# Optimization experiments

Measured on AMD Instinct MI355X. Metric: run time of the kernel, lower is better.

The kernel has to match this reference:

```python
import jax, jax.numpy as jnp
import numpy as np

B, N, DIM = 2, 512, 512
HEADS, DIM_HEAD, MAX_LEN = 8, 64, 1024


def _skew(QEr):
    # pad last dim on the left by 1, reshape (n, n+1) -> (n+1, n), drop first row
    padded = jnp.pad(QEr, ((0, 0), (0, 0), (0, 0), (1, 0)))
    b, h, r, c = padded.shape
    return padded.reshape(b, h, c, r)[:, :, 1:, :]


def _fft_multiply_parallel(A, x):
    # A: [b,h,n,n] decay matrix; x: [b,h,n,d]
    b, h, n, d = x.shape
    # y = [last column of A, first row of A] -> [b,h,2n]
    y = jnp.concatenate([A[:, :, :, -1], A[:, :, 0, :]], axis=-1)
    v = jnp.concatenate([x, jnp.zeros_like(x)], axis=-2)  # zero-pad rows n -> 2n
    # Faithful to the original torch code: fftn over ALL axes (incl. batch/head),
    # then ifft over the LAST axis only, then slice back to n rows.
    H = jnp.fft.fftn(y)[:, :, :, None] * jnp.fft.fftn(v)
    return jnp.fft.ifft(H)[:, :, :n, :]


def _forward(x, Wq, Wk, Wv, Er):
    b, n, _ = x.shape

    def split_heads(t):
        return t.reshape(b, n, HEADS, DIM_HEAD).transpose(0, 2, 1, 3)  # [b,h,n,d]

    q = split_heads(x @ Wq)
    k = split_heads(x @ Wk)
    v = split_heads(x @ Wv)
    # global (Frobenius) norm over the full tensor, as torch.norm(t)
    q = q / jnp.linalg.norm(q)
    k = k / jnp.linalg.norm(k)
    q_ = jax.nn.elu(q)
    k_ = jax.nn.elu(k)

    Er_t = Er[MAX_LEN - n:, :].T        # [d, n]
    QEr = q @ Er_t                       # [b,h,n,n]
    c = jnp.exp(_skew(QEr))              # relative-position decay, [b,h,n,n]

    a_1 = jnp.einsum('bhnx,bhny->bhnxy', k_, v).reshape(b, HEADS, n, DIM_HEAD * DIM_HEAD)
    d_2 = _fft_multiply_parallel(c, k_)                                   # [b,h,n,d] complex
    d_1 = _fft_multiply_parallel(c, a_1).reshape(b, HEADS, n, DIM_HEAD, DIM_HEAD)

    top = jnp.einsum('bhnx,bhnyz->bhnz', q_, d_1)    # complex [b,h,n,d]
    bottom = jnp.einsum('bhnx,bhny->bhny', q_, d_2)  # complex [b,h,n,d]
    return top / bottom


def setup_inputs() -> dict:
    key = jax.random.key(0)
    k1, k2, k3, k4, k5 = jax.random.split(key, 5)
    s = jnp.float32(1.0 / np.sqrt(DIM))
    return {
        'x': jax.random.normal(k1, (B, N, DIM), dtype=jnp.float32),
        'Wq': jax.random.normal(k2, (DIM, HEADS * DIM_HEAD), dtype=jnp.float32) * s,
        'Wk': jax.random.normal(k3, (DIM, HEADS * DIM_HEAD), dtype=jnp.float32) * s,
        'Wv': jax.random.normal(k4, (DIM, HEADS * DIM_HEAD), dtype=jnp.float32) * s,
        'Er': jax.random.normal(k5, (MAX_LEN, DIM_HEAD), dtype=jnp.float32),
    }


def reference(x, Wq, Wk, Wv, Er):
    return _forward(x, Wq, Wk, Wv, Er)
```

## Files before the change

kernel.cpp:

```cpp
#include <hip/hip_runtime.h>
#include <math.h>


#define DIMX 512
#define NPOS 512
#define PADIDX(m) ((m) + ((m) >> 4))

typedef unsigned short ushort_t;
typedef unsigned int uint_t;
typedef __bf16 bf16x8 __attribute__((ext_vector_type(8)));
typedef float floatx4 __attribute__((ext_vector_type(4)));

static __device__ inline ushort_t f2bf(float f) {
    uint_t u = __float_as_uint(f);
    u = u + 0x7FFFu + ((u >> 16) & 1u);
    return (ushort_t)(u >> 16);
}
static __device__ inline float bf2f(ushort_t h) {
    return __uint_as_float(((uint_t)h) << 16);
}

#define BFLY(lo, hi, tw) do {                                   \
    const float sr_ = (lo).x - (hi).x, si_ = (lo).y - (hi).y;   \
    (lo).x += (hi).x; (lo).y += (hi).y;                         \
    (hi).x = sr_ * (tw).x - si_ * (tw).y;                       \
    (hi).y = sr_ * (tw).y + si_ * (tw).x;                       \
} while (0)

__global__ __launch_bounds__(256)
void conv_kernel(const float* __restrict__ x,
                 const float* __restrict__ Wk, const float* __restrict__ Wv,
                 ushort_t* __restrict__ xh, ushort_t* __restrict__ xl,
                 ushort_t* __restrict__ wth, ushort_t* __restrict__ wtl,
                 float2* __restrict__ twd)
{
    const int blk = blockIdx.x;
    const int t = threadIdx.x;
    if (blk < 512) {
        const int idx4 = blk * 256 + t;
        const float4 v = ((const float4*)x)[idx4];
        const float vf[4] = {v.x, v.y, v.z, v.w};
        ushort_t h[4], l[4];
        #pragma unroll
        for (int e = 0; e < 4; ++e) {
            h[e] = f2bf(vf[e]);
            l[e] = f2bf(vf[e] - bf2f(h[e]));
        }
        const ushort4 hv4 = make_ushort4(h[0], h[1], h[2], h[3]);
        const ushort4 lv4 = make_ushort4(l[0], l[1], l[2], l[3]);
        *(ushort4*)(xh + (size_t)idx4 * 4) = hv4;
        *(ushort4*)(xl + (size_t)idx4 * 4) = lv4;
    } else if (blk < 1024) {
        __shared__ float tile[32][33];
        const int b2 = blk - 512;
        const int s  = b2 >> 8;
        const int kt = (b2 >> 4) & 15;
        const int nt = b2 & 15;
        const int c  = t & 31, r4 = t >> 5;
        const float* __restrict__ W = s ? Wv : Wk;
        #pragma unroll
        for (int i = 0; i < 4; ++i) {
            const int row = r4 + i * 8;
            tile[row][c] = W[(size_t)(kt * 32 + row) * 512 + nt * 32 + c];
        }
        __syncthreads();
        #pragma unroll
        for (int i = 0; i < 4; ++i) {
            const int nl = r4 + i * 8;
            const float v = tile[c][nl];
            const ushort_t h = f2bf(v);
            const ushort_t l = f2bf(v - bf2f(h));
            const size_t o = (size_t)(s * 512 + nt * 32 + nl) * 512 + kt * 32 + c;
            wth[o] = h;
            wtl[o] = l;
        }
    } else {
        const int jj = (blk - 1024) * 256 + t;
        double s, cc;
        sincos(-6.2831853071795864769 * (double)jj / 1024.0, &s, &cc);
        twd[jj] = make_float2((float)cc, (float)s);
    }
}

__global__ __launch_bounds__(256)
void gemm_mfma_kernel(const ushort_t* __restrict__ xh, const ushort_t* __restrict__ xl,
                      const ushort_t* __restrict__ wth, const ushort_t* __restrict__ wtl,
                      float* __restrict__ K, float* __restrict__ V,
                      float* __restrict__ partials)
{
    const int blk = blockIdx.x;
    const int ct = blk >> 5;
    const int rt = blk & 31;
    const int t = threadIdx.x;
    const int w = t >> 6, lane = t & 63;
    const int qd = lane >> 4, lm = lane & 15;
    const int mrow  = rt * 32 + (w >> 1) * 16 + lm;
    const int ncol0 = ct * 64 + (w & 1) * 32;
    const size_t aoff  = (size_t)mrow * 512 + qd * 8;
    const size_t boff0 = (size_t)(ncol0 + lm) * 512 + qd * 8;
    const size_t boff1 = (size_t)(ncol0 + 16 + lm) * 512 + qd * 8;

    floatx4 acc0 = {0.f, 0.f, 0.f, 0.f};
    floatx4 acc1 = {0.f, 0.f, 0.f, 0.f};

    #pragma unroll
    for (int ks = 0; ks < 16; ++ks) {
        const int k0 = ks * 32;
        const bf16x8 Ah  = *(const bf16x8*)&xh [aoff  + k0];
        const bf16x8 Al  = *(const bf16x8*)&xl [aoff  + k0];
        const bf16x8 B0h = *(const bf16x8*)&wth[boff0 + k0];
        const bf16x8 B0l = *(const bf16x8*)&wtl[boff0 + k0];
        const bf16x8 B1h = *(const bf16x8*)&wth[boff1 + k0];
        const bf16x8 B1l = *(const bf16x8*)&wtl[boff1 + k0];
        acc0 = __builtin_amdgcn_mfma_f32_16x16x32_bf16(Ah, B0h, acc0, 0, 0, 0);
        acc0 = __builtin_amdgcn_mfma_f32_16x16x32_bf16(Ah, B0l, acc0, 0, 0, 0);
        acc0 = __builtin_amdgcn_mfma_f32_16x16x32_bf16(Al, B0h, acc0, 0, 0, 0);
        acc1 = __builtin_amdgcn_mfma_f32_16x16x32_bf16(Ah, B1h, acc1, 0, 0, 0);
        acc1 = __builtin_amdgcn_mfma_f32_16x16x32_bf16(Ah, B1l, acc1, 0, 0, 0);
        acc1 = __builtin_amdgcn_mfma_f32_16x16x32_bf16(Al, B1h, acc1, 0, 0, 0);
    }

    __shared__ float red[4];
    float ss = 0.f;
    const int orow0 = rt * 32 + (w >> 1) * 16 + qd * 4;
    float* __restrict__ O = (ct < 8) ? K : V;
    const int cb = (ct < 8) ? 0 : 512;
    const int c0 = ncol0 + lm - cb;
    #pragma unroll
    for (int r = 0; r < 4; ++r) {
        const size_t row = orow0 + r;
        const float v0 = acc0[r], v1 = acc1[r];
        O[row * 512 + c0]      = v0;
        O[row * 512 + c0 + 16] = v1;
        if (ct < 8) ss += v0 * v0 + v1 * v1;
    }
    #pragma unroll
    for (int off = 32; off > 0; off >>= 1)
        ss += __shfl_down(ss, off, 64);
    if (lane == 0) red[w] = ss;
    __syncthreads();
    if (t == 0) partials[blk] = red[0] + red[1] + red[2] + red[3];
}

__device__ __constant__ float C8[8] = {
    1.f, 0.70710678118654752440f, 0.f, -0.70710678118654752440f,
   -1.f, -0.70710678118654752440f, 0.f, 0.70710678118654752440f };
__device__ __constant__ float S8[8] = {
    0.f, -0.70710678118654752440f, -1.f, -0.70710678118654752440f,
    0.f,  0.70710678118654752440f,  1.f,  0.70710678118654752440f };

__global__ __launch_bounds__(256)
void stage1_kernel(const float* __restrict__ K,
                   const float* __restrict__ V,
                   const float* __restrict__ partials,
                   float2* __restrict__ Gk,
                   float2* __restrict__ Gp)
{
    const int m = blockIdx.x;
    const int t = threadIdx.x;
    __shared__ float kk[2][8][64];
    __shared__ float pp[2][8][64];
    __shared__ float skp[16][4];
    __shared__ float sk[2][8];
    __shared__ float sred[4];

    float p = partials[t] + partials[t + 256];
    #pragma unroll
    for (int off = 32; off > 0; off >>= 1)
        p += __shfl_down(p, off, 64);
    if ((t & 63) == 0) sred[t >> 6] = p;
    __syncthreads();
    const float scale = (float)(1.0 / sqrt((double)sred[0] + (double)sred[1] +
                                           (double)sred[2] + (double)sred[3]));

    {
        const int e0 = t * 4;
        const int b = e0 >> 9, rem = e0 & 511, h = rem >> 6, z = rem & 63;
        const size_t src = (size_t)(b * 512 + m) * DIMX + h * 64 + z;
        const float4 kv4 = *(const float4*)&K[src];
        const float4 vv4 = *(const float4*)&V[src];
        const float kf[4] = {kv4.x, kv4.y, kv4.z, kv4.w};
        const float vf[4] = {vv4.x, vv4.y, vv4.z, vv4.w};
        #pragma unroll
        for (int e = 0; e < 4; ++e) {
            const float kv = kf[e] * scale;
            kk[b][h][z + e] = kv > 0.f ? kv : expm1f(kv);
            pp[b][h][z + e] = vf[e];
        }
    }
    __syncthreads();
    if (t < 64) {
        const int bh = t >> 2, q = t & 3;
        float s = 0.f;
        #pragma unroll
        for (int zz = 0; zz < 16; ++zz) s += kk[bh >> 3][bh & 7][q * 16 + zz];
        skp[bh][q] = s;
    }
    __syncthreads();
    if (t < 16) sk[t >> 3][t & 7] = skp[t][0] + skp[t][1] + skp[t][2] + skp[t][3];
    __syncthreads();

    for (int e2 = t; e2 < 512; e2 += 256) {
        const int be = e2 >> 5;
        const int zp = e2 & 31;
        const int beta = be >> 3, eta = be & 7;
        float kr[2] = {0.f, 0.f}, ki[2] = {0.f, 0.f};
        float pr[2] = {0.f, 0.f}, pim[2] = {0.f, 0.f};
        #pragma unroll
        for (int b = 0; b < 2; ++b) {
            const float sgn = (beta & b) ? -1.f : 1.f;
            #pragma unroll
            for (int h = 0; h < 8; ++h) {
                const int ph = (eta * h) & 7;
                const float cr = C8[ph], ci = S8[ph];
                const float skv = sk[b][h];
                #pragma unroll
                for (int zz = 0; zz < 2; ++zz) {
                    const int z = zp * 2 + zz;
                    const float a = kk[b][h][z] * sgn;
                    kr[zz] = fmaf(a, cr, kr[zz]);
                    ki[zz] = fmaf(a, ci, ki[zz]);
                    const float p2 = (pp[b][h][z] * skv) * sgn;
                    pr[zz]  = fmaf(p2, cr, pr[zz]);
                    pim[zz] = fmaf(p2, ci, pim[zz]);
                }
            }
        }
        const float4 rk = make_float4(kr[0], ki[0], kr[1], ki[1]);
        const float4 rp = make_float4(pr[0], pim[0], pr[1], pim[1]);
        const size_t o = ((size_t)be * NPOS + m) * 64 + zp * 2;
        *(float4*)&Gk[o] = rk;
        *(float4*)&Gp[o] = rp;
    }
}

__global__ __launch_bounds__(256)
void fft_div_kernel(const float2* __restrict__ Gk,
                    const float2* __restrict__ Gp,
                    const float2* __restrict__ twd,
                    float* __restrict__ out, int out_cplx)
{
    const int blk = blockIdx.x;
    const int j  = blk & 7;
    const int l  = (blk >> 3) & 3;
    const int be = blk >> 5;
    const int zg = j * 4 + l;
    const int t  = threadIdx.x;

    __shared__ float2 g[4][1088];
    __shared__ float2 w[544];

    for (int jj = t; jj < 512; jj += 256)
        w[PADIDX(jj)] = twd[jj];
    __syncthreads();

    for (int e = t; e < 1024; e += 256) {
        const int a = e >> 9;
        const int m = e & 511;
        const float4 v4 = *(const float4*)&(a ? Gp : Gk)[((size_t)be * NPOS + m) * 64 + zg * 2];
        const float2 v0 = make_float2(v4.x, v4.y);
        const float2 v1 = make_float2(v4.z, v4.w);
        const float2 tw = w[PADIDX(m)];
        g[a * 2 + 0][PADIDX(m)] = v0;
        g[a * 2 + 1][PADIDX(m)] = v1;
        g[a * 2 + 0][PADIDX(m + 512)] = make_float2(v0.x * tw.x - v0.y * tw.y,
                                                    v0.x * tw.y + v0.y * tw.x);
        g[a * 2 + 1][PADIDX(m + 512)] = make_float2(v1.x * tw.x - v1.y * tw.y,
                                                    v1.x * tw.y + v1.y * tw.x);
    }
    __syncthreads();

    const int wv   = t >> 6;
    const int lane = t & 63;

    #pragma unroll
    for (int q = 0; q < 2; ++q) {
        const int arr = wv;
        const int h   = q;
        const int jo  = lane;
        float2 f[8];
        #pragma unroll
        for (int k = 0; k < 8; ++k)
            f[k] = g[arr][PADIDX(h * 512 + jo + k * 64)];
        #pragma unroll
        for (int k = 0; k < 4; ++k) {
            const float2 tw = w[PADIDX(2 * jo + 128 * k)];
            BFLY(f[k], f[k + 4], tw);
        }
        {
            const float2 tw0 = w[PADIDX(4 * jo)];
            const float2 tw1 = w[PADIDX(4 * jo + 256)];
            BFLY(f[0], f[2], tw0); BFLY(f[1], f[3], tw1);
            BFLY(f[4], f[6], tw0); BFLY(f[5], f[7], tw1);
        }
        {
            const float2 tw = w[PADIDX(8 * jo)];
            BFLY(f[0], f[1], tw); BFLY(f[2], f[3], tw);
            BFLY(f[4], f[5], tw); BFLY(f[6], f[7], tw);
        }
        #pragma unroll
        for (int k = 0; k < 8; ++k)
            g[arr][PADIDX(h * 512 + jo + k * 64)] = f[k];
    }

    #pragma unroll
    for (int q = 0; q < 2; ++q) {
        const int arr = wv;
        const int b64 = q * 8 + (lane >> 3);
        const int jo  = lane & 7;
        const int e0  = b64 * 64 + jo;
        float2 f[8];
        #pragma unroll
        for (int k = 0; k < 8; ++k)
            f[k] = g[arr][PADIDX(e0 + 8 * k)];
        #pragma unroll
        for (int k = 0; k < 4; ++k) {
            const float2 tw = w[PADIDX(16 * jo + 128 * k)];
            BFLY(f[k], f[k + 4], tw);
        }
        {
            const float2 tw0 = w[PADIDX(32 * jo)];
            const float2 tw1 = w[PADIDX(32 * jo + 256)];
            BFLY(f[0], f[2], tw0); BFLY(f[1], f[3], tw1);
            BFLY(f[4], f[6], tw0); BFLY(f[5], f[7], tw1);
        }
        {
            const float2 tw = w[PADIDX(64 * jo)];
            BFLY(f[0], f[1], tw); BFLY(f[2], f[3], tw);
            BFLY(f[4], f[5], tw); BFLY(f[6], f[7], tw);
        }
        #pragma unroll
        for (int k = 0; k < 8; ++k)
            g[arr][PADIDX(e0 + 8 * k)] = f[k];
    }

    #pragma unroll
    for (int q = 0; q < 2; ++q) {
        const int arr = wv;
        const int b8  = q * 64 + lane;
        const int e0  = b8 * 8;
        float2 f[8];
        #pragma unroll
        for (int k = 0; k < 8; ++k)
            f[k] = g[arr][PADIDX(e0 + k)];
        BFLY(f[0], f[4], w[PADIDX(0)]);
        BFLY(f[1], f[5], w[PADIDX(128)]);
        BFLY(f[2], f[6], w[PADIDX(256)]);
        BFLY(f[3], f[7], w[PADIDX(384)]);
        {
            const float2 tw0 = w[PADIDX(0)];
            const float2 tw1 = w[PADIDX(256)];
            BFLY(f[0], f[2], tw0); BFLY(f[1], f[3], tw1);
            BFLY(f[4], f[6], tw0); BFLY(f[5], f[7], tw1);
        }
        f[0].x += f[1].x; f[0].y += f[1].y;
        f[2].x += f[3].x; f[2].y += f[3].y;
        f[4].x += f[5].x; f[4].y += f[5].y;
        f[6].x += f[7].x; f[6].y += f[7].y;
        g[arr][PADIDX(e0 + 0)] = f[0];
        g[arr][PADIDX(e0 + 2)] = f[2];
        g[arr][PADIDX(e0 + 4)] = f[4];
        g[arr][PADIDX(e0 + 6)] = f[6];
    }
    __syncthreads();

    for (int e2 = t; e2 < 512; e2 += 256) {
        const int i  = e2;
        const int pi = PADIDX(2 * i);
        const int mu = (int)(__brev((unsigned)i) >> 23);
        float4 res;
        #pragma unroll
        for (int zi = 0; zi < 2; ++zi) {
            const float2 D  = g[zi][pi];
            const float2 Nm = g[2 + zi][pi];
            const float inv = 1.f / (D.x * D.x + D.y * D.y);
            const float rr = (Nm.x * D.x + Nm.y * D.y) * inv;
            const float ri = (Nm.y * D.x - Nm.x * D.y) * inv;
            if (zi == 0) { res.x = rr; res.y = ri; }
            else         { res.z = rr; res.w = ri; }
        }
        const size_t o = ((size_t)be * NPOS + mu) * 64 + zg * 2;
        if (out_cplx) {
            *(float4*)&((float2*)out)[o] = res;
        } else {
            out[o]     = res.x;
            out[o + 1] = res.z;
        }
    }
}

__global__ __launch_bounds__(256)
void gemm_kv_kernel(const float* __restrict__ x,
                    const float* __restrict__ Wk,
                    const float* __restrict__ Wv,
                    float* __restrict__ K,
                    float* __restrict__ V,
                    float* __restrict__ partials)
{
    const int blk  = blockIdx.x;
    const int sel  = (blk >> 2) & 1;
    const int cg2  = blk & 3;
    const int rt   = blk >> 3;
    const int row0 = rt * 16;
    const int col0 = cg2 * 128;
    const int t    = threadIdx.x;
    const int tc   = t & 31;
    const int tr   = t >> 5;
    const float* __restrict__ W   = sel ? Wv : Wk;
    float* __restrict__       Out = sel ? V  : K;

    __shared__ float xs[16][DIMX];
    __shared__ float red[4];

    #pragma unroll
    for (int jj = 0; jj < 8; ++jj) {
        const int f = t + jj * 256;
        const int row = f >> 7, c4 = f & 127;
        *(float4*)&xs[row][c4 * 4] = *(const float4*)&x[(size_t)(row0 + row) * DIMX + c4 * 4];
    }
    __syncthreads();

    const float* Wb = W + col0 + tc * 4;
    float4 wA[8], wB[8];
    #pragma unroll
    for (int jj = 0; jj < 8; ++jj) wA[jj] = *(const float4*)&Wb[(size_t)(jj) * DIMX];
    #pragma unroll
    for (int jj = 0; jj < 8; ++jj) wB[jj] = *(const float4*)&Wb[(size_t)(8 + jj) * DIMX];

    float acc[2][4] = {{0,0,0,0},{0,0,0,0}};
    const int r0 = tr * 2;

    #define COMPUTE_CHUNK(WREG, CH)                                            \
        {   float4 xv0a = *(const float4*)&xs[r0][(CH) * 8];                   \
            float4 xv0b = *(const float4*)&xs[r0][(CH) * 8 + 4];               \
            float4 xv1a = *(const float4*)&xs[r0 + 1][(CH) * 8];               \
            float4 xv1b = *(const float4*)&xs[r0 + 1][(CH) * 8 + 4];           \
            _Pragma("unroll")                                                  \
            for (int kk = 0; kk < 4; ++kk) {                                   \
                const float x0 = (&xv0a.x)[kk], x1 = (&xv1a.x)[kk];            \
                _Pragma("unroll")                                              \
                for (int cc = 0; cc < 4; ++cc) {                               \
                    acc[0][cc] = fmaf(x0, (&WREG[kk].x)[cc], acc[0][cc]);      \
                    acc[1][cc] = fmaf(x1, (&WREG[kk].x)[cc], acc[1][cc]);      \
                } }                                                            \
            _Pragma("unroll")                                                  \
            for (int kk = 0; kk < 4; ++kk) {                                   \
                const float x0 = (&xv0b.x)[kk], x1 = (&xv1b.x)[kk];            \
                _Pragma("unroll")                                              \
                for (int cc = 0; cc < 4; ++cc) {                               \
                    acc[0][cc] = fmaf(x0, (&WREG[kk + 4].x)[cc], acc[0][cc]);  \
                    acc[1][cc] = fmaf(x1, (&WREG[kk + 4].x)[cc], acc[1][cc]);  \
                } } }

    for (int ch = 0; ch < 64; ch += 2) {
        COMPUTE_CHUNK(wA, ch)
        if (ch < 62) {
            #pragma unroll
            for (int jj = 0; jj < 8; ++jj)
                wA[jj] = *(const float4*)&Wb[(size_t)((ch + 2) * 8 + jj) * DIMX];
        }
        COMPUTE_CHUNK(wB, ch + 1)
        if (ch < 62) {
            #pragma unroll
            for (int jj = 0; jj < 8; ++jj)
                wB[jj] = *(const float4*)&Wb[(size_t)((ch + 3) * 8 + jj) * DIMX];
        }
    }
    #undef COMPUTE_CHUNK

    float ss = 0.f;
    #pragma unroll
    for (int i = 0; i < 2; ++i) {
        const int row = row0 + r0 + i;
        const float4 o = make_float4(acc[i][0], acc[i][1], acc[i][2], acc[i][3]);
        *(float4*)&Out[(size_t)row * DIMX + col0 + tc * 4] = o;
        ss += o.x * o.x + o.y * o.y + o.z * o.z + o.w * o.w;
    }
    if (sel == 0) {
        #pragma unroll
        for (int off = 32; off > 0; off >>= 1)
            ss += __shfl_down(ss, off, 64);
        if ((t & 63) == 0) red[t >> 6] = ss;
        __syncthreads();
        if (t == 0) partials[blk] = red[0] + red[1] + red[2] + red[3];
    } else {
        if (t == 0) partials[blk] = 0.f;
    }
}

__global__ __launch_bounds__(256)
void mdft_fallback_kernel(const float2* __restrict__ Gk,
                          const float2* __restrict__ Gp,
                          float* __restrict__ out,
                          int out_cplx)
{
    const int blk = blockIdx.x;
    const int be = blk >> 6, z = blk & 63;
    const int t = threadIdx.x;
    __shared__ float2 gk[512];
    __shared__ float2 gp[512];
    __shared__ float2 w[1024];

    for (int m = t; m < 512; m += 256) {
        const size_t idx = ((size_t)be * NPOS + m) * 64 + z;
        gk[m] = Gk[idx];
        gp[m] = Gp[idx];
    }
    for (int jj = t; jj < 1024; jj += 256) {
        double s, c;
        sincos(-6.2831853071795864769 * (double)jj / 1024.0, &s, &c);
        w[jj] = make_float2((float)c, (float)s);
    }
    __syncthreads();

    #pragma unroll
    for (int half = 0; half < 2; ++half) {
        const int mu = t + half * 256;
        double dr = 0.0, di = 0.0, nr = 0.0, ni = 0.0;
        int idx = 0;
        for (int m = 0; m < 512; ++m) {
            const float2 tw = w[idx];
            idx = (idx + mu) & 1023;
            const float2 a = gk[m];
            dr += (double)(a.x * tw.x - a.y * tw.y);
            di += (double)(a.x * tw.y + a.y * tw.x);
            const float2 p2 = gp[m];
            nr += (double)(p2.x * tw.x - p2.y * tw.y);
            ni += (double)(p2.x * tw.y + p2.y * tw.x);
        }
        const double dmag = dr * dr + di * di;
        const double orr = (nr * dr + ni * di) / dmag;
        const double oii = (ni * dr - nr * di) / dmag;
        const size_t o = ((size_t)be * NPOS + mu) * 64 + z;
        if (out_cplx) {
            out[2 * o]     = (float)orr;
            out[2 * o + 1] = (float)oii;
        } else {
            out[o] = (float)orr;
        }
    }
}

extern "C" void kernel_launch(void* const* d_in, const int* in_sizes, int n_in,
                              void* d_out, int out_size, void* d_ws, size_t ws_size,
                              hipStream_t stream)
{
    const float* x  = (const float*)d_in[0];
    const float* Wk = (const float*)d_in[2];
    const float* Wv = (const float*)d_in[3];
    float* out = (float*)d_out;

    char* ws = (char*)d_ws;
    float*  K    = (float*)(ws);
    float*  V    = (float*)(ws + (size_t)2097152);
    float2* Gk   = (float2*)(ws + (size_t)4194304);
    float*  part = (float*)(ws + (size_t)8388608);
    const int out_cplx = (out_size >= 2 * 2 * 8 * 512 * 64) ? 1 : 0;

    const bool ws_big = (ws_size >= (size_t)20971520);
    float2* Gp = ws_big ? (float2*)(ws + (size_t)8390656)
                        : (float2*)d_out;

    if (ws_big) {
        ushort_t* xh  = (ushort_t*)(ws + (size_t)16777216);
        ushort_t* xl  = (ushort_t*)(ws + (size_t)17825792);
        ushort_t* wth = (ushort_t*)(ws + (size_t)18874368);
        ushort_t* wtl = (ushort_t*)(ws + (size_t)19922944);
        float2*   twd = (float2*)(ws + (size_t)12584960);
        hipLaunchKernelGGL(conv_kernel, dim3(1026), dim3(256), 0, stream,
                           x, Wk, Wv, xh, xl, wth, wtl, twd);
        hipLaunchKernelGGL(gemm_mfma_kernel, dim3(512), dim3(256), 0, stream,
                           xh, xl, wth, wtl, K, V, part);
        hipLaunchKernelGGL(stage1_kernel, dim3(512), dim3(256), 0, stream,
                           K, V, part, Gk, Gp);
        hipLaunchKernelGGL(fft_div_kernel, dim3(512), dim3(256), 0, stream,
                           Gk, Gp, twd, out, out_cplx);
    } else {
        hipLaunchKernelGGL(gemm_kv_kernel, dim3(512), dim3(256), 0, stream,
                           x, Wk, Wv, K, V, part);
        hipLaunchKernelGGL(stage1_kernel, dim3(512), dim3(256), 0, stream,
                           K, V, part, Gk, Gp);
        hipLaunchKernelGGL(mdft_fallback_kernel, dim3(1024), dim3(256), 0, stream,
                           Gk, Gp, out, out_cplx);
    }
}
```

Measured before the change: 105.4 us.

## Stage GEMM weight tiles in LDS with async loads; fuse FFT pre-twiddle

The projection GEMM now brings each block's shared weight tile into double-buffered LDS through global_load_lds. All four waves read the tile from there, where before each wave loaded it redundantly from global memory, and the wave-to-tile mapping is reorganised to match. The FFT-divide kernel no longer stores a pre-twiddled upper half at load time. The first radix stage now reads the lower half and applies the twiddle in registers, handling the twiddled half first so the in-place writes are safe. This removes one LDS write pass and one barrier, at the cost of added barriers per k-step in the GEMM.

After: 100.1 us. 5.0% less time.

```diff
diff --git a/kernel.cpp b/kernel.cpp
--- a/kernel.cpp
+++ b/kernel.cpp
@@ -94,38 +94,62 @@
     const int t = threadIdx.x;
     const int w = t >> 6, lane = t & 63;
     const int qd = lane >> 4, lm = lane & 15;
-    const int mrow  = rt * 32 + (w >> 1) * 16 + lm;
-    const int ncol0 = ct * 64 + (w & 1) * 32;
-    const size_t aoff  = (size_t)mrow * 512 + qd * 8;
-    const size_t boff0 = (size_t)(ncol0 + lm) * 512 + qd * 8;
-    const size_t boff1 = (size_t)(ncol0 + 16 + lm) * 512 + qd * 8;
+
+    const int mrow = rt * 32 + (w & 1) * 16 + lm;
+    const int wcol = (w >> 1) * 32;
+    const size_t aoff = (size_t)mrow * 512 + qd * 8;
+
+    __shared__ __align__(16) ushort_t Bs[2][2][8][64][8];
+    __shared__ float red[4];
+
+    #define STAGE(buf_, k0_)                                                     \
+    {                                                                            \
+        _Pragma("unroll")                                                        \
+        for (int i = 0; i < 4; ++i) {                                            \
+            const int seg = w * 4 + i;                                           \
+            const int arr_ = seg >> 3, kq_ = seg & 7;                            \
+            const ushort_t* src_ = (arr_ ? wtl : wth)                            \
+                + (size_t)(ct * 64 + lane) * 512 + (k0_) + kq_ * 8;              \
+            __builtin_amdgcn_global_load_lds(                                    \
+                (const __attribute__((address_space(1))) uint_t*)src_,           \
+                (__attribute__((address_space(3))) uint_t*)&Bs[buf_][arr_][kq_][0][0], \
+                16, 0, 0);                                                       \
+        }                                                                        \
+    }
 
     floatx4 acc0 = {0.f, 0.f, 0.f, 0.f};
     floatx4 acc1 = {0.f, 0.f, 0.f, 0.f};
 
-    #pragma unroll
-    for (int ks = 0; ks < 16; ++ks) {
-        const int k0 = ks * 32;
-        const bf16x8 Ah  = *(const bf16x8*)&xh [aoff  + k0];
-        const bf16x8 Al  = *(const bf16x8*)&xl [aoff  + k0];
-        const bf16x8 B0h = *(const bf16x8*)&wth[boff0 + k0];
-        const bf16x8 B0l = *(const bf16x8*)&wtl[boff0 + k0];
-        const bf16x8 B1h = *(const bf16x8*)&wth[boff1 + k0];
-        const bf16x8 B1l = *(const bf16x8*)&wtl[boff1 + k0];
-        acc0 = __builtin_amdgcn_mfma_f32_16x16x32_bf16(Ah, B0h, acc0, 0, 0, 0);
-        acc0 = __builtin_amdgcn_mfma_f32_16x16x32_bf16(Ah, B0l, acc0, 0, 0, 0);
-        acc0 = __builtin_amdgcn_mfma_f32_16x16x32_bf16(Al, B0h, acc0, 0, 0, 0);
-        acc1 = __builtin_amdgcn_mfma_f32_16x16x32_bf16(Ah, B1h, acc1, 0, 0, 0);
-        acc1 = __builtin_amdgcn_mfma_f32_16x16x32_bf16(Ah, B1l, acc1, 0, 0, 0);
-        acc1 = __builtin_amdgcn_mfma_f32_16x16x32_bf16(Al, B1h, acc1, 0, 0, 0);
-    }
-
-    __shared__ float red[4];
+    STAGE(0, 0)
+    for (int ks = 0; ks < 8; ++ks) {
+        __syncthreads();
+        const int buf = ks & 1;
+        const int k0 = ks * 64;
+        if (ks < 7) STAGE(buf ^ 1, k0 + 64)
+        #pragma unroll
+        for (int s2 = 0; s2 < 2; ++s2) {
+            const bf16x8 Ah = *(const bf16x8*)&xh[aoff + k0 + s2 * 32];
+            const bf16x8 Al = *(const bf16x8*)&xl[aoff + k0 + s2 * 32];
+            const int kq = s2 * 4 + qd;
+            const bf16x8 B0h = *(const bf16x8*)Bs[buf][0][kq][wcol + lm];
+            const bf16x8 B0l = *(const bf16x8*)Bs[buf][1][kq][wcol + lm];
+            const bf16x8 B1h = *(const bf16x8*)Bs[buf][0][kq][wcol + 16 + lm];
+            const bf16x8 B1l = *(const bf16x8*)Bs[buf][1][kq][wcol + 16 + lm];
+            acc0 = __builtin_amdgcn_mfma_f32_16x16x32_bf16(Ah, B0h, acc0, 0, 0, 0);
+            acc0 = __builtin_amdgcn_mfma_f32_16x16x32_bf16(Ah, B0l, acc0, 0, 0, 0);
+            acc0 = __builtin_amdgcn_mfma_f32_16x16x32_bf16(Al, B0h, acc0, 0, 0, 0);
+            acc1 = __builtin_amdgcn_mfma_f32_16x16x32_bf16(Ah, B1h, acc1, 0, 0, 0);
+            acc1 = __builtin_amdgcn_mfma_f32_16x16x32_bf16(Ah, B1l, acc1, 0, 0, 0);
+            acc1 = __builtin_amdgcn_mfma_f32_16x16x32_bf16(Al, B1h, acc1, 0, 0, 0);
+        }
+    }
+    #undef STAGE
+
     float ss = 0.f;
-    const int orow0 = rt * 32 + (w >> 1) * 16 + qd * 4;
+    const int orow0 = rt * 32 + (w & 1) * 16 + qd * 4;
     float* __restrict__ O = (ct < 8) ? K : V;
     const int cb = (ct < 8) ? 0 : 512;
-    const int c0 = ncol0 + lm - cb;
+    const int c0 = ct * 64 + wcol + lm - cb;
     #pragma unroll
     for (int r = 0; r < 4; ++r) {
         const size_t row = orow0 + r;
@@ -252,21 +276,12 @@
 
     for (int jj = t; jj < 512; jj += 256)
         w[PADIDX(jj)] = twd[jj];
-    __syncthreads();
-
     for (int e = t; e < 1024; e += 256) {
         const int a = e >> 9;
         const int m = e & 511;
         const float4 v4 = *(const float4*)&(a ? Gp : Gk)[((size_t)be * NPOS + m) * 64 + zg * 2];
-        const float2 v0 = make_float2(v4.x, v4.y);
-        const float2 v1 = make_float2(v4.z, v4.w);
-        const float2 tw = w[PADIDX(m)];
-        g[a * 2 + 0][PADIDX(m)] = v0;
-        g[a * 2 + 1][PADIDX(m)] = v1;
-        g[a * 2 + 0][PADIDX(m + 512)] = make_float2(v0.x * tw.x - v0.y * tw.y,
-                                                    v0.x * tw.y + v0.y * tw.x);
-        g[a * 2 + 1][PADIDX(m + 512)] = make_float2(v1.x * tw.x - v1.y * tw.y,
-                                                    v1.x * tw.y + v1.y * tw.x);
+        g[a * 2 + 0][PADIDX(m)] = make_float2(v4.x, v4.y);
+        g[a * 2 + 1][PADIDX(m)] = make_float2(v4.z, v4.w);
     }
     __syncthreads();
 
@@ -274,14 +289,22 @@
     const int lane = t & 63;
 
     #pragma unroll
-    for (int q = 0; q < 2; ++q) {
+    for (int qh = 0; qh < 2; ++qh) {
+        const int hh  = 1 - qh;
         const int arr = wv;
-        const int h   = q;
         const int jo  = lane;
         float2 f[8];
         #pragma unroll
         for (int k = 0; k < 8; ++k)
-            f[k] = g[arr][PADIDX(h * 512 + jo + k * 64)];
+            f[k] = g[arr][PADIDX(jo + k * 64)];
+        if (hh == 1) {
+            #pragma unroll
+            for (int k = 0; k < 8; ++k) {
+                const float2 tw = w[PADIDX(jo + k * 64)];
+                f[k] = make_float2(f[k].x * tw.x - f[k].y * tw.y,
+                                   f[k].x * tw.y + f[k].y * tw.x);
+            }
+        }
         #pragma unroll
         for (int k = 0; k < 4; ++k) {
             const float2 tw = w[PADIDX(2 * jo + 128 * k)];
@@ -300,7 +323,7 @@
         }
         #pragma unroll
         for (int k = 0; k < 8; ++k)
-            g[arr][PADIDX(h * 512 + jo + k * 64)] = f[k];
+            g[arr][PADIDX(hh * 512 + jo + k * 64)] = f[k];
     }
 
     #pragma unroll
```
